# Performance work log

Hardware: AMD Instinct MI355X
Metric: run time of the kernel (lower is better)

## Reference

```python
import jax, jax.numpy as jnp
import numpy as np

BS, N, D = 4, 512, 128

def setup_inputs() -> dict:
    key = jax.random.key(0)
    ks = jax.random.split(key, 8)
    s = 1.0 / np.sqrt(D)
    return {
        "x":  jax.random.normal(ks[0], (BS, N, D), dtype=jnp.float32),
        "Wq": jax.random.normal(ks[1], (D, D), dtype=jnp.float32) * s,
        "bq": jax.random.normal(ks[2], (D,), dtype=jnp.float32) * s,
        "Wk": jax.random.normal(ks[3], (D, D), dtype=jnp.float32) * s,
        "bk": jax.random.normal(ks[4], (D,), dtype=jnp.float32) * s,
        "Wv": jax.random.normal(ks[5], (D, D), dtype=jnp.float32) * s,
        "bv": jax.random.normal(ks[6], (D,), dtype=jnp.float32) * s,
        "pos_bias": jax.random.normal(ks[7], (N, N), dtype=jnp.float32) * 0.1,
    }

def reference(x, Wq, bq, Wk, bk, Wv, bv, pos_bias):
    # Linear projections (torch Linear: x @ W^T + b)
    q = jax.nn.sigmoid(jnp.einsum('bnd,ed->bne', x, Wq) + bq)   # [B,N,D]
    k = jnp.einsum('bnd,ed->bne', x, Wk) + bk                   # [B,N,D]
    v = jnp.einsum('bnd,ed->bne', x, Wv) + bv                   # [B,N,D]
    # scores[b,t,j,d] = k[b,j,d] + pos_bias[t,j]  (O(n^2 d) intermediate)
    s = k[:, None, :, :] + pos_bias[None, :, :, None]           # [B,N,N,D]
    m = jnp.max(s, axis=2, keepdims=True)                       # stabilizer
    e = jnp.exp(s - m)                                          # [B,N,N,D]
    num = jnp.einsum('btjd,bjd->btd', e, v)                     # [B,N,D]
    den = jnp.sum(e, axis=2)                                    # [B,N,D]
    return q * (num / den)
```

## Files before the change

kernel.cpp:

```cpp
#include <hip/hip_runtime.h>

#define BATCH 4
#define SEQ   512
#define DIM   128

typedef _Float16 half8 __attribute__((ext_vector_type(8)));
typedef _Float16 half4 __attribute__((ext_vector_type(4)));
typedef float    f32x4 __attribute__((ext_vector_type(4)));

static __device__ __forceinline__ half8 cvt_h8(const float4 a, const float4 b) {
    half8 h;
    h[0] = (_Float16)a.x; h[1] = (_Float16)a.y; h[2] = (_Float16)a.z; h[3] = (_Float16)a.w;
    h[4] = (_Float16)b.x; h[5] = (_Float16)b.y; h[6] = (_Float16)b.z; h[7] = (_Float16)b.w;
    return h;
}

__global__ __launch_bounds__(256) void k_proj(
    const float* __restrict__ x,
    const float* __restrict__ Wq, const float* __restrict__ bq,
    const float* __restrict__ Wk, const float* __restrict__ bk,
    const float* __restrict__ Wv, const float* __restrict__ bv,
    const float* __restrict__ pos,
    float* __restrict__ qoutT, _Float16* __restrict__ ekk,
    _Float16* __restrict__ ep_h)
{
    const int tid  = threadIdx.x;
    const int lane = tid & 63;
    const int wave = tid >> 6;
    const int l15  = lane & 15;
    const int quad = lane >> 4;

    const int n0 = (blockIdx.x & 7) * 16;
    const int m0 = (blockIdx.x >> 3) * 64 + wave * 16;

    const float* xa = x  + (m0 + l15) * DIM + quad * 8;
    const float* wq = Wq + (n0 + l15) * DIM + quad * 8;
    const float* wk = Wk + (n0 + l15) * DIM + quad * 8;
    const float* wv = Wv + (n0 + l15) * DIM + quad * 8;

    f32x4 aq = {0.f, 0.f, 0.f, 0.f};
    f32x4 ak = {0.f, 0.f, 0.f, 0.f};
    f32x4 av = {0.f, 0.f, 0.f, 0.f};

#pragma unroll
    for (int ks = 0; ks < 4; ++ks) {
        const half8 a  = cvt_h8(*(const float4*)(xa + ks * 32),
                                *(const float4*)(xa + ks * 32 + 4));
        const half8 b0 = cvt_h8(*(const float4*)(wq + ks * 32),
                                *(const float4*)(wq + ks * 32 + 4));
        const half8 b1 = cvt_h8(*(const float4*)(wk + ks * 32),
                                *(const float4*)(wk + ks * 32 + 4));
        const half8 b2 = cvt_h8(*(const float4*)(wv + ks * 32),
                                *(const float4*)(wv + ks * 32 + 4));
        aq = __builtin_amdgcn_mfma_f32_16x16x32_f16(a, b0, aq, 0, 0, 0);
        ak = __builtin_amdgcn_mfma_f32_16x16x32_f16(a, b1, ak, 0, 0, 0);
        av = __builtin_amdgcn_mfma_f32_16x16x32_f16(a, b2, av, 0, 0, 0);
    }

    const int c   = n0 + l15;
    const float bqv = bq[c];
    const float bkv = bk[c];
    const float bvv = bv[c];

    const int mrow = m0 + quad * 4;
    const int b    = mrow >> 9;
    const int tok  = mrow & 511;

    half4 eh, evh;
    float4 q4;
#pragma unroll
    for (int r = 0; r < 4; ++r) {
        const float e  = __expf(ak[r] + bkv);
        const float vv = av[r] + bvv;
        eh[r]  = (_Float16)e;
        evh[r] = (_Float16)(e * vv);
        ((float*)&q4)[r] = 1.f / (1.f + __expf(-(aq[r] + bqv)));
    }
    *(half4*)(ekk + ((b * 256) + 2 * c + 0) * SEQ + tok) = eh;
    *(half4*)(ekk + ((b * 256) + 2 * c + 1) * SEQ + tok) = evh;
    *(float4*)(qoutT + ((b * DIM) + c) * SEQ + tok) = q4;

    const int i = (blockIdx.x * 256 + tid) * 4;
    const float4 p = *(const float4*)(pos + i);
    half4 h;
    h[0] = (_Float16)__expf(p.x); h[1] = (_Float16)__expf(p.y);
    h[2] = (_Float16)__expf(p.z); h[3] = (_Float16)__expf(p.w);
    *(half4*)(ep_h + i) = h;
}

__global__ __launch_bounds__(512, 2) void k_aft(
    const _Float16* __restrict__ ekk,
    const _Float16* __restrict__ ep_h,
    const float* __restrict__ qoutT,
    float* __restrict__ out)
{
    const int tid  = threadIdx.x;
    const int lane = tid & 63;
    const int wave = tid >> 6;
    const int l15  = lane & 15;
    const int quad = lane >> 4;
    const int wm   = wave & 1;
    const int wn   = wave >> 1;

    const int b  = blockIdx.x >> 6;
    const int m0 = (((blockIdx.x >> 3) & 7) * 32) + wm * 16;
    const int t0 = ((blockIdx.x & 7) * 64) + wn * 16;

    const _Float16* arow = ekk  + ((b * 256) + m0 + l15) * SEQ + quad * 8;
    const _Float16* brow = ep_h + (t0 + l15) * SEQ + quad * 8;

    f32x4 acc = {0.f, 0.f, 0.f, 0.f};

#pragma unroll
    for (int ks = 0; ks < 16; ++ks) {
        const half8 a  = *(const half8*)(arow + ks * 32);
        const half8 bf = *(const half8*)(brow + ks * 32);
        acc = __builtin_amdgcn_mfma_f32_16x16x32_f16(a, bf, acc, 0, 0, 0);
    }

    const int d0 = (m0 + quad * 4) >> 1;
    const int t  = t0 + l15;
    const float q0 = qoutT[((b * DIM) + d0) * SEQ + t];
    const float q1 = qoutT[((b * DIM) + d0 + 1) * SEQ + t];
    float2 o;
    o.x = q0 * acc[1] / acc[0];
    o.y = q1 * acc[3] / acc[2];
    *(float2*)(out + ((b * SEQ) + t) * DIM + d0) = o;
}

extern "C" void kernel_launch(void* const* d_in, const int* in_sizes, int n_in,
                              void* d_out, int out_size, void* d_ws, size_t ws_size,
                              hipStream_t stream) {
    const float* x   = (const float*)d_in[0];
    const float* Wq  = (const float*)d_in[1];
    const float* bq  = (const float*)d_in[2];
    const float* Wk  = (const float*)d_in[3];
    const float* bk  = (const float*)d_in[4];
    const float* Wv  = (const float*)d_in[5];
    const float* bv  = (const float*)d_in[6];
    const float* pos = (const float*)d_in[7];

    float* outp = (float*)d_out;
    char*  ws   = (char*)d_ws;

    _Float16* ep_h  = (_Float16*)(ws);
    _Float16* ekk   = (_Float16*)(ws + (512 << 10));
    float*    qoutT = (float*)   (ws + (1536 << 10));

    k_proj<<<256, 256, 0, stream>>>(x, Wq, bq, Wk, bk, Wv, bv, pos, qoutT, ekk, ep_h);
    k_aft <<<256, 512, 0, stream>>>(ekk, ep_h, qoutT, outp);
}
```

Baseline: 80.91 us.

## Fuse projections, exp, and AFT matmul into a single kernel with LDS staging

Replaces the two-kernel pipeline with one fused kernel. Each block recomputes exp(k) and exp(k)*v for its batch's 64 dims, stages them in swizzled LDS together with exp(pos_bias) rows, and runs the AFT matmul from LDS. The q sigmoid is computed per output with scalar dot products. This removes the workspace round trip and the second launch, but recomputes the K/V projection redundantly across t-tiles.

```diff
diff --git a/kernel.cpp b/kernel.cpp
--- a/kernel.cpp
+++ b/kernel.cpp
@@ -15,117 +15,121 @@
     return h;
 }
 
-__global__ __launch_bounds__(256) void k_proj(
+#define IDXA(m, jj) ((m) * 128 + ((jj) ^ ((((m) >> 1) & 7) << 3)))
+#define IDXB(t, jj) ((t) * 128 + ((jj) ^ (((t) & 7) << 3)))
+
+__global__ __launch_bounds__(512, 2) void k_fused(
     const float* __restrict__ x,
     const float* __restrict__ Wq, const float* __restrict__ bq,
     const float* __restrict__ Wk, const float* __restrict__ bk,
     const float* __restrict__ Wv, const float* __restrict__ bv,
     const float* __restrict__ pos,
-    float* __restrict__ qoutT, _Float16* __restrict__ ekk,
-    _Float16* __restrict__ ep_h)
+    float* __restrict__ out)
 {
+    __shared__ _Float16 ldsA[128 * 128];
+    __shared__ _Float16 ldsB[16 * 128];
+
     const int tid  = threadIdx.x;
     const int lane = tid & 63;
-    const int wave = tid >> 6;
+    const int w    = tid >> 6;
     const int l15  = lane & 15;
     const int quad = lane >> 4;
 
-    const int n0 = (blockIdx.x & 7) * 16;
-    const int m0 = (blockIdx.x >> 3) * 64 + wave * 16;
+    const int bid   = blockIdx.x;
+    const int b     = bid >> 6;
+    const int tt    = (bid & 63) >> 1;
+    const int b2    = bid & 1;
+    const int t0    = tt * 16;
+    const int dbase = b2 * 64;
 
-    const float* xa = x  + (m0 + l15) * DIM + quad * 8;
-    const float* wq = Wq + (n0 + l15) * DIM + quad * 8;
-    const float* wk = Wk + (n0 + l15) * DIM + quad * 8;
-    const float* wv = Wv + (n0 + l15) * DIM + quad * 8;
+    const int dt = w & 3;
+    const int nh = w >> 2;
 
-    f32x4 aq = {0.f, 0.f, 0.f, 0.f};
-    f32x4 ak = {0.f, 0.f, 0.f, 0.f};
-    f32x4 av = {0.f, 0.f, 0.f, 0.f};
-
+    const float* wkr = Wk + (dbase + dt * 16 + l15) * DIM + quad * 8;
+    const float* wvr = Wv + (dbase + dt * 16 + l15) * DIM + quad * 8;
+    half8 wkf[4], wvf[4];
 #pragma unroll
     for (int ks = 0; ks < 4; ++ks) {
-        const half8 a  = cvt_h8(*(const float4*)(xa + ks * 32),
-                                *(const float4*)(xa + ks * 32 + 4));
-        const half8 b0 = cvt_h8(*(const float4*)(wq + ks * 32),
-                                *(const float4*)(wq + ks * 32 + 4));
-        const half8 b1 = cvt_h8(*(const float4*)(wk + ks * 32),
-                                *(const float4*)(wk + ks * 32 + 4));
-        const half8 b2 = cvt_h8(*(const float4*)(wv + ks * 32),
-                                *(const float4*)(wv + ks * 32 + 4));
-        aq = __builtin_amdgcn_mfma_f32_16x16x32_f16(a, b0, aq, 0, 0, 0);
-        ak = __builtin_amdgcn_mfma_f32_16x16x32_f16(a, b1, ak, 0, 0, 0);
-        av = __builtin_amdgcn_mfma_f32_16x16x32_f16(a, b2, av, 0, 0, 0);
+        wkf[ks] = cvt_h8(*(const float4*)(wkr + ks * 32), *(const float4*)(wkr + ks * 32 + 4));
+        wvf[ks] = cvt_h8(*(const float4*)(wvr + ks * 32), *(const float4*)(wvr + ks * 32 + 4));
     }
+    const int de = dbase + dt * 16 + quad * 4;
+    const float4 bk4 = *(const float4*)(bk + de);
+    const float4 bv4 = *(const float4*)(bv + de);
 
-    const int c   = n0 + l15;
-    const float bqv = bq[c];
-    const float bkv = bk[c];
-    const float bvv = bv[c];
-
-    const int mrow = m0 + quad * 4;
-    const int b    = mrow >> 9;
-    const int tok  = mrow & 511;
-
-    half4 eh, evh;
-    float4 q4;
-#pragma unroll
-    for (int r = 0; r < 4; ++r) {
-        const float e  = __expf(ak[r] + bkv);
-        const float vv = av[r] + bvv;
-        eh[r]  = (_Float16)e;
-        evh[r] = (_Float16)(e * vv);
-        ((float*)&q4)[r] = 1.f / (1.f + __expf(-(aq[r] + bqv)));
-    }
-    *(half4*)(ekk + ((b * 256) + 2 * c + 0) * SEQ + tok) = eh;
-    *(half4*)(ekk + ((b * 256) + 2 * c + 1) * SEQ + tok) = evh;
-    *(float4*)(qoutT + ((b * DIM) + c) * SEQ + tok) = q4;
-
-    const int i = (blockIdx.x * 256 + tid) * 4;
-    const float4 p = *(const float4*)(pos + i);
-    half4 h;
-    h[0] = (_Float16)__expf(p.x); h[1] = (_Float16)__expf(p.y);
-    h[2] = (_Float16)__expf(p.z); h[3] = (_Float16)__expf(p.w);
-    *(half4*)(ep_h + i) = h;
-}
-
-__global__ __launch_bounds__(512, 2) void k_aft(
-    const _Float16* __restrict__ ekk,
-    const _Float16* __restrict__ ep_h,
-    const float* __restrict__ qoutT,
-    float* __restrict__ out)
-{
-    const int tid  = threadIdx.x;
-    const int lane = tid & 63;
-    const int wave = tid >> 6;
-    const int l15  = lane & 15;
-    const int quad = lane >> 4;
-    const int wm   = wave & 1;
-    const int wn   = wave >> 1;
-
-    const int b  = blockIdx.x >> 6;
-    const int m0 = (((blockIdx.x >> 3) & 7) * 32) + wm * 16;
-    const int t0 = ((blockIdx.x & 7) * 64) + wn * 16;
-
-    const _Float16* arow = ekk  + ((b * 256) + m0 + l15) * SEQ + quad * 8;
-    const _Float16* brow = ep_h + (t0 + l15) * SEQ + quad * 8;
+    const float* xb = x + b * SEQ * DIM;
 
     f32x4 acc = {0.f, 0.f, 0.f, 0.f};
 
+    for (int ch = 0; ch < 4; ++ch) {
 #pragma unroll
-    for (int ks = 0; ks < 16; ++ks) {
-        const half8 a  = *(const half8*)(arow + ks * 32);
-        const half8 bf = *(const half8*)(brow + ks * 32);
-        acc = __builtin_amdgcn_mfma_f32_16x16x32_f16(a, bf, acc, 0, 0, 0);
+        for (int nt = 0; nt < 4; ++nt) {
+            const int jj16 = (nh * 4 + nt) * 16;
+            const int jrow = ch * 128 + jj16 + l15;
+            const float* xr = xb + jrow * DIM + quad * 8;
+            f32x4 dk = {0.f, 0.f, 0.f, 0.f};
+            f32x4 dv = {0.f, 0.f, 0.f, 0.f};
+#pragma unroll
+            for (int ks = 0; ks < 4; ++ks) {
+                const half8 xf = cvt_h8(*(const float4*)(xr + ks * 32),
+                                        *(const float4*)(xr + ks * 32 + 4));
+                dk = __builtin_amdgcn_mfma_f32_16x16x32_f16(wkf[ks], xf, dk, 0, 0, 0);
+                dv = __builtin_amdgcn_mfma_f32_16x16x32_f16(wvf[ks], xf, dv, 0, 0, 0);
+            }
+            const int jj = jj16 + l15;
+#pragma unroll
+            for (int r = 0; r < 4; ++r) {
+                const float e  = __expf(dk[r] + bk4[r]);
+                const float vv = dv[r] + bv4[r];
+                const int m0 = 2 * (dt * 16 + quad * 4 + r);
+                ldsA[IDXA(m0,     jj)] = (_Float16)e;
+                ldsA[IDXA(m0 + 1, jj)] = (_Float16)(e * vv);
+            }
+        }
+        {
+            const int tl = tid >> 5;
+            const int jj = (tid & 31) * 4;
+            const float4 p = *(const float4*)(pos + (t0 + tl) * SEQ + ch * 128 + jj);
+            half4 h;
+            h[0] = (_Float16)__expf(p.x); h[1] = (_Float16)__expf(p.y);
+            h[2] = (_Float16)__expf(p.z); h[3] = (_Float16)__expf(p.w);
+            *(half4*)&ldsA[0 - 0 + 0], (void)0;
+            *(half4*)&ldsB[IDXB(tl, jj)] = h;
+        }
+        __syncthreads();
+        {
+            const int mrow = 16 * w + l15;
+#pragma unroll
+            for (int ks = 0; ks < 4; ++ks) {
+                const int kk = ks * 32 + quad * 8;
+                const half8 af = *(const half8*)&ldsA[IDXA(mrow, kk)];
+                const half8 bf = *(const half8*)&ldsB[IDXB(l15, kk)];
+                acc = __builtin_amdgcn_mfma_f32_16x16x32_f16(af, bf, acc, 0, 0, 0);
+            }
+        }
+        __syncthreads();
     }
 
-    const int d0 = (m0 + quad * 4) >> 1;
+    const int d0 = dbase + 8 * w + 2 * quad;
     const int t  = t0 + l15;
-    const float q0 = qoutT[((b * DIM) + d0) * SEQ + t];
-    const float q1 = qoutT[((b * DIM) + d0 + 1) * SEQ + t];
+    const float* xr = xb + t * DIM;
+    const float* w0 = Wq + d0 * DIM;
+    const float* w1 = w0 + DIM;
+    float s0 = 0.f, s1 = 0.f;
+#pragma unroll
+    for (int k4 = 0; k4 < 32; ++k4) {
+        const float4 xv = *(const float4*)(xr + k4 * 4);
+        const float4 a0 = *(const float4*)(w0 + k4 * 4);
+        const float4 a1 = *(const float4*)(w1 + k4 * 4);
+        s0 += xv.x * a0.x + xv.y * a0.y + xv.z * a0.z + xv.w * a0.w;
+        s1 += xv.x * a1.x + xv.y * a1.y + xv.z * a1.z + xv.w * a1.w;
+    }
+    const float q0 = 1.f / (1.f + __expf(-(s0 + bq[d0])));
+    const float q1 = 1.f / (1.f + __expf(-(s1 + bq[d0 + 1])));
     float2 o;
     o.x = q0 * acc[1] / acc[0];
     o.y = q1 * acc[3] / acc[2];
-    *(float2*)(out + ((b * SEQ) + t) * DIM + d0) = o;
+    *(float2*)(out + (b * SEQ + t) * DIM + d0) = o;
 }
 
 extern "C" void kernel_launch(void* const* d_in, const int* in_sizes, int n_in,
@@ -140,13 +144,7 @@
     const float* bv  = (const float*)d_in[6];
     const float* pos = (const float*)d_in[7];
 
-    float* outp = (float*)d_out;
-    char*  ws   = (char*)d_ws;
+    (void)d_ws; (void)ws_size;
 
-    _Float16* ep_h  = (_Float16*)(ws);
-    _Float16* ekk   = (_Float16*)(ws + (512 << 10));
-    float*    qoutT = (float*)   (ws + (1536 << 10));
-
-    k_proj<<<256, 256, 0, stream>>>(x, Wq, bq, Wk, bk, Wv, bv, pos, qoutT, ekk, ep_h);
-    k_aft <<<256, 512, 0, stream>>>(ekk, ep_h, qoutT, outp);
+    k_fused<<<256, 512, 0, stream>>>(x, Wq, bq, Wk, bk, Wv, bv, pos, (float*)d_out);
 }
```

Result: slower. 113.3 us (+40.0%).

## Fuse projection and AFT kernels into one cooperative launch with grid sync

Applied to the files above, without the earlier changes.

Merges the two kernels into a single cooperative kernel of 256 blocks × 512 threads. Half the waves compute K/V, the other half compute Q and exp(pos_bias), then a grid-wide sync separates this from the AFT matmul phase, which is remapped to one 16x16 tile per wave. The aim is to remove the second launch and its gap. In exchange it adds a grid barrier and the cooperative-launch overhead, and it changes the work split of the projection phase. An unused leftover argument array is kept.

```diff
diff --git a/kernel.cpp b/kernel.cpp
--- a/kernel.cpp
+++ b/kernel.cpp
@@ -1,4 +1,7 @@
 #include <hip/hip_runtime.h>
+#include <hip/hip_cooperative_groups.h>
+
+namespace cg = cooperative_groups;
 
 #define BATCH 4
 #define SEQ   512
@@ -15,117 +18,118 @@
     return h;
 }
 
-__global__ __launch_bounds__(256) void k_proj(
+__global__ __launch_bounds__(512, 2) void k_coop(
     const float* __restrict__ x,
     const float* __restrict__ Wq, const float* __restrict__ bq,
     const float* __restrict__ Wk, const float* __restrict__ bk,
     const float* __restrict__ Wv, const float* __restrict__ bv,
     const float* __restrict__ pos,
-    float* __restrict__ qoutT, _Float16* __restrict__ ekk,
-    _Float16* __restrict__ ep_h)
+    _Float16* __restrict__ ekk, _Float16* __restrict__ ep_h,
+    float* __restrict__ qoutT, float* __restrict__ out)
 {
     const int tid  = threadIdx.x;
     const int lane = tid & 63;
-    const int wave = tid >> 6;
+    const int w    = tid >> 6;
     const int l15  = lane & 15;
     const int quad = lane >> 4;
+    const int bid  = blockIdx.x;
 
-    const int n0 = (blockIdx.x & 7) * 16;
-    const int m0 = (blockIdx.x >> 3) * 64 + wave * 16;
+    const int n0 = (bid & 7) * 16;
+    const int c  = n0 + l15;
 
-    const float* xa = x  + (m0 + l15) * DIM + quad * 8;
-    const float* wq = Wq + (n0 + l15) * DIM + quad * 8;
-    const float* wk = Wk + (n0 + l15) * DIM + quad * 8;
-    const float* wv = Wv + (n0 + l15) * DIM + quad * 8;
+    if (w < 4) {
+        const int mglob = (bid >> 3) * 64 + w * 16;
+        const float* xa  = x  + (mglob + l15) * DIM + quad * 8;
+        const float* wkr = Wk + c * DIM + quad * 8;
+        const float* wvr = Wv + c * DIM + quad * 8;
 
-    f32x4 aq = {0.f, 0.f, 0.f, 0.f};
-    f32x4 ak = {0.f, 0.f, 0.f, 0.f};
-    f32x4 av = {0.f, 0.f, 0.f, 0.f};
+        f32x4 ak = {0.f, 0.f, 0.f, 0.f};
+        f32x4 av = {0.f, 0.f, 0.f, 0.f};
+#pragma unroll
+        for (int ks = 0; ks < 4; ++ks) {
+            const half8 a  = cvt_h8(*(const float4*)(xa + ks * 32),
+                                    *(const float4*)(xa + ks * 32 + 4));
+            const half8 b1 = cvt_h8(*(const float4*)(wkr + ks * 32),
+                                    *(const float4*)(wkr + ks * 32 + 4));
+            const half8 b2 = cvt_h8(*(const float4*)(wvr + ks * 32),
+                                    *(const float4*)(wvr + ks * 32 + 4));
+            ak = __builtin_amdgcn_mfma_f32_16x16x32_f16(a, b1, ak, 0, 0, 0);
+            av = __builtin_amdgcn_mfma_f32_16x16x32_f16(a, b2, av, 0, 0, 0);
+        }
+        const float bkv = bk[c];
+        const float bvv = bv[c];
+        const int mrow = mglob + quad * 4;
+        const int b    = mrow >> 9;
+        const int tok  = mrow & 511;
+        half4 eh, evh;
+#pragma unroll
+        for (int r = 0; r < 4; ++r) {
+            const float e  = __expf(ak[r] + bkv);
+            const float vv = av[r] + bvv;
+            eh[r]  = (_Float16)e;
+            evh[r] = (_Float16)(e * vv);
+        }
+        *(half4*)(ekk + ((b * 256) + 2 * c + 0) * SEQ + tok) = eh;
+        *(half4*)(ekk + ((b * 256) + 2 * c + 1) * SEQ + tok) = evh;
+    } else {
+        const int mglob = (bid >> 3) * 64 + (w - 4) * 16;
+        const float* xa  = x  + (mglob + l15) * DIM + quad * 8;
+        const float* wqr = Wq + c * DIM + quad * 8;
 
+        f32x4 aq = {0.f, 0.f, 0.f, 0.f};
 #pragma unroll
-    for (int ks = 0; ks < 4; ++ks) {
-        const half8 a  = cvt_h8(*(const float4*)(xa + ks * 32),
-                                *(const float4*)(xa + ks * 32 + 4));
-        const half8 b0 = cvt_h8(*(const float4*)(wq + ks * 32),
-                                *(const float4*)(wq + ks * 32 + 4));
-        const half8 b1 = cvt_h8(*(const float4*)(wk + ks * 32),
-                                *(const float4*)(wk + ks * 32 + 4));
-        const half8 b2 = cvt_h8(*(const float4*)(wv + ks * 32),
-                                *(const float4*)(wv + ks * 32 + 4));
-        aq = __builtin_amdgcn_mfma_f32_16x16x32_f16(a, b0, aq, 0, 0, 0);
-        ak = __builtin_amdgcn_mfma_f32_16x16x32_f16(a, b1, ak, 0, 0, 0);
-        av = __builtin_amdgcn_mfma_f32_16x16x32_f16(a, b2, av, 0, 0, 0);
+        for (int ks = 0; ks < 4; ++ks) {
+            const half8 a  = cvt_h8(*(const float4*)(xa + ks * 32),
+                                    *(const float4*)(xa + ks * 32 + 4));
+            const half8 b0 = cvt_h8(*(const float4*)(wqr + ks * 32),
+                                    *(const float4*)(wqr + ks * 32 + 4));
+            aq = __builtin_amdgcn_mfma_f32_16x16x32_f16(a, b0, aq, 0, 0, 0);
+        }
+        const float bqv = bq[c];
+        const int mrow = mglob + quad * 4;
+        const int b    = mrow >> 9;
+        const int tok  = mrow & 511;
+        float4 q4;
+#pragma unroll
+        for (int r = 0; r < 4; ++r)
+            ((float*)&q4)[r] = 1.f / (1.f + __expf(-(aq[r] + bqv)));
+        *(float4*)(qoutT + ((b * DIM) + c) * SEQ + tok) = q4;
+
+        const int i = (bid * 256 + (w - 4) * 64 + lane) * 4;
+        const float4 p = *(const float4*)(pos + i);
+        half4 h;
+        h[0] = (_Float16)__expf(p.x); h[1] = (_Float16)__expf(p.y);
+        h[2] = (_Float16)__expf(p.z); h[3] = (_Float16)__expf(p.w);
+        *(half4*)(ep_h + i) = h;
     }
 
-    const int c   = n0 + l15;
-    const float bqv = bq[c];
-    const float bkv = bk[c];
-    const float bvv = bv[c];
+    cg::this_grid().sync();
 
-    const int mrow = m0 + quad * 4;
-    const int b    = mrow >> 9;
-    const int tok  = mrow & 511;
+    const int widx = bid * 8 + w;
+    const int b2   = widx >> 9;
+    const int r2   = widx & 511;
+    const int m0   = (r2 >> 5) * 16;
+    const int t0   = (r2 & 31) * 16;
 
-    half4 eh, evh;
-    float4 q4;
-#pragma unroll
-    for (int r = 0; r < 4; ++r) {
-        const float e  = __expf(ak[r] + bkv);
-        const float vv = av[r] + bvv;
-        eh[r]  = (_Float16)e;
-        evh[r] = (_Float16)(e * vv);
-        ((float*)&q4)[r] = 1.f / (1.f + __expf(-(aq[r] + bqv)));
-    }
-    *(half4*)(ekk + ((b * 256) + 2 * c + 0) * SEQ + tok) = eh;
-    *(half4*)(ekk + ((b * 256) + 2 * c + 1) * SEQ + tok) = evh;
-    *(float4*)(qoutT + ((b * DIM) + c) * SEQ + tok) = q4;
-
-    const int i = (blockIdx.x * 256 + tid) * 4;
-    const float4 p = *(const float4*)(pos + i);
-    half4 h;
-    h[0] = (_Float16)__expf(p.x); h[1] = (_Float16)__expf(p.y);
-    h[2] = (_Float16)__expf(p.z); h[3] = (_Float16)__expf(p.w);
-    *(half4*)(ep_h + i) = h;
-}
-
-__global__ __launch_bounds__(512, 2) void k_aft(
-    const _Float16* __restrict__ ekk,
-    const _Float16* __restrict__ ep_h,
-    const float* __restrict__ qoutT,
-    float* __restrict__ out)
-{
-    const int tid  = threadIdx.x;
-    const int lane = tid & 63;
-    const int wave = tid >> 6;
-    const int l15  = lane & 15;
-    const int quad = lane >> 4;
-    const int wm   = wave & 1;
-    const int wn   = wave >> 1;
-
-    const int b  = blockIdx.x >> 6;
-    const int m0 = (((blockIdx.x >> 3) & 7) * 32) + wm * 16;
-    const int t0 = ((blockIdx.x & 7) * 64) + wn * 16;
-
-    const _Float16* arow = ekk  + ((b * 256) + m0 + l15) * SEQ + quad * 8;
+    const _Float16* arow = ekk  + ((b2 * 256) + m0 + l15) * SEQ + quad * 8;
     const _Float16* brow = ep_h + (t0 + l15) * SEQ + quad * 8;
 
     f32x4 acc = {0.f, 0.f, 0.f, 0.f};
-
 #pragma unroll
     for (int ks = 0; ks < 16; ++ks) {
-        const half8 a  = *(const half8*)(arow + ks * 32);
+        const half8 af = *(const half8*)(arow + ks * 32);
         const half8 bf = *(const half8*)(brow + ks * 32);
-        acc = __builtin_amdgcn_mfma_f32_16x16x32_f16(a, bf, acc, 0, 0, 0);
+        acc = __builtin_amdgcn_mfma_f32_16x16x32_f16(af, bf, acc, 0, 0, 0);
     }
 
     const int d0 = (m0 + quad * 4) >> 1;
     const int t  = t0 + l15;
-    const float q0 = qoutT[((b * DIM) + d0) * SEQ + t];
-    const float q1 = qoutT[((b * DIM) + d0 + 1) * SEQ + t];
+    const float q0 = qoutT[((b2 * DIM) + d0) * SEQ + t];
+    const float q1 = qoutT[((b2 * DIM) + d0 + 1) * SEQ + t];
     float2 o;
     o.x = q0 * acc[1] / acc[0];
     o.y = q1 * acc[3] / acc[2];
-    *(float2*)(out + ((b * SEQ) + t) * DIM + d0) = o;
+    *(float2*)(out + ((b2 * SEQ) + t) * DIM + d0) = o;
 }
 
 extern "C" void kernel_launch(void* const* d_in, const int* in_sizes, int n_in,
@@ -136,9 +140,10 @@
     const float* bq  = (const float*)d_in[2];
     const float* Wk  = (const float*)d_in[3];
     const float* bk  = (const float*)d_in[4];
+    const float* bv_ = (const float*)d_in[6];
     const float* Wv  = (const float*)d_in[5];
-    const float* bv  = (const float*)d_in[6];
     const float* pos = (const float*)d_in[7];
+    const float* bk_ = bk;
 
     float* outp = (float*)d_out;
     char*  ws   = (char*)d_ws;
@@ -147,6 +152,18 @@
     _Float16* ekk   = (_Float16*)(ws + (512 << 10));
     float*    qoutT = (float*)   (ws + (1536 << 10));
 
-    k_proj<<<256, 256, 0, stream>>>(x, Wq, bq, Wk, bk, Wv, bv, pos, qoutT, ekk, ep_h);
-    k_aft <<<256, 512, 0, stream>>>(ekk, ep_h, qoutT, outp);
+    void* args[] = {
+        (void*)&x, (void*)&Wq, (void*)&bq, (void*)&bk_, (void*)&bk,
+        (void*)&Wv, (void*)&bv_, (void*)&pos,
+        (void*)&ekk, (void*)&ep_h, (void*)&qoutT, (void*)&outp
+    };
+    const float* Wk_ = Wk;
+    void* args_fixed[] = {
+        (void*)&x, (void*)&Wq, (void*)&bq, (void*)&Wk_, (void*)&bk,
+        (void*)&Wv, (void*)&bv_, (void*)&pos,
+        (void*)&ekk, (void*)&ep_h, (void*)&qoutT, (void*)&outp
+    };
+    (void)args;
+    hipLaunchCooperativeKernel((const void*)k_coop, dim3(256), dim3(512),
+                               args_fixed, 0, stream);
 }
```

Result: slower. 122.8 us (+51.7%).
